# Performance work log

Measured on AMD Instinct MI355X. Metric: run time of the kernel, lower is better.

## Reference

```python
import jax, jax.numpy as jnp
import numpy as np

EPS_PROJ = 0.004   # float32 branch of _project
EPS_MIN = 1e-15


def _poincare_linear(x, weight_v, weight_g, bias, c):
    c = c.reshape(())
    rc = jnp.sqrt(c)
    # z_unit: column-normalized weight (weight_v / ||weight_v||_col)
    z_unit = weight_v / jnp.maximum(jnp.linalg.norm(weight_v, axis=0), EPS_MIN)  # [in, out]
    # unidirectional Poincare MLR
    drcr = 2.0 * rc * bias                                  # [out]
    rcx = rc * x                                            # [N, in]
    cx2 = jnp.sum(rcx * rcx, axis=-1, keepdims=True)        # [N, 1]
    num = 2.0 * (rcx @ z_unit) * jnp.cosh(drcr) - (1.0 + cx2) * jnp.sinh(drcr)
    mlr = 2.0 * weight_g / rc * jnp.arcsinh(num / jnp.maximum(1.0 - cx2, EPS_MIN))  # [N, out]
    # map back to the ball: sinh, then gyro-half map
    y = jnp.sinh(rc * mlr) / rc
    y = y / (1.0 + jnp.sqrt(1.0 + c * jnp.sum(y * y, axis=-1, keepdims=True)))
    # _project onto ball of curvature k = -c
    k = -c
    maxnorm = (1.0 - EPS_PROJ) / jnp.sqrt(jnp.maximum(jnp.abs(k), EPS_MIN))
    maxnorm = jnp.where(k < 0, maxnorm, jnp.float32(1e15))
    norm = jnp.maximum(jnp.linalg.norm(y, axis=-1, keepdims=True), EPS_MIN)
    return jnp.where(norm > maxnorm, y / norm * maxnorm, y)


def setup_inputs() -> dict:
    key = jax.random.key(0)
    k1, k2, k3 = jax.random.split(key, 3)
    N, IN, OUT = 32768, 1024, 1024
    # points strictly inside the unit Poincare ball (||x|| ~ 0.64)
    x = jax.random.normal(k1, (N, IN), dtype=jnp.float32) * 0.02
    std = (2.0 * IN * OUT) ** (-0.5)
    weight_v = jax.random.normal(k2, (IN, OUT), dtype=jnp.float32) * std
    weight_g = jax.random.uniform(k3, (OUT,), dtype=jnp.float32, minval=0.5, maxval=1.5) * std * (IN ** 0.5)
    bias = jnp.zeros((OUT,), dtype=jnp.float32)
    c = jnp.ones((1,), dtype=jnp.float32)
    return {"x": x, "weight_v": weight_v, "weight_g": weight_g, "bias": bias, "c": c}


def reference(x, weight_v, weight_g, bias, c):
    return _poincare_linear(x, weight_v, weight_g, bias, c)
```

## Files before the change

kernel.cpp:

```cpp
#include <hip/hip_runtime.h>

#define K_DIM 1024
#define N_DIM 1024

typedef short v8s __attribute__((ext_vector_type(8)));
typedef float v4f __attribute__((ext_vector_type(4)));

__device__ __forceinline__ unsigned int bf16_rne(float f) {
    unsigned int u = __float_as_uint(f);
    u += 0x7FFFu + ((u >> 16) & 1u);
    return u >> 16;
}

__global__ void sumsq_cols(const float* __restrict__ wv, float* __restrict__ colss) {
    __shared__ float red[4][64];
    const int t = threadIdx.x;
    const int cj = t & 63, rr = t >> 6;
    const int col = (blockIdx.x & 15) * 64 + cj;
    const int k0 = (blockIdx.x >> 4) * 128 + rr * 32;
    float ss = 0.f;
#pragma unroll 8
    for (int i = 0; i < 32; ++i) {
        float v = wv[(size_t)(k0 + i) * N_DIM + col];
        ss = fmaf(v, v, ss);
    }
    red[rr][cj] = ss;
    __syncthreads();
    if (rr == 0) atomicAdd(&colss[col], red[0][cj] + red[1][cj] + red[2][cj] + red[3][cj]);
}

__global__ void finalize_cols(const float* __restrict__ colss, const float* __restrict__ wg,
                              const float* __restrict__ bias, const float* __restrict__ cptr,
                              float* __restrict__ colinv, float* __restrict__ coshd,
                              float* __restrict__ sinhd, float* __restrict__ gfac) {
    const int col = blockIdx.x * 256 + threadIdx.x;
    const float rc = sqrtf(cptr[0]);
    colinv[col] = 1.0f / fmaxf(sqrtf(colss[col]), 1e-15f);
    float d = 2.0f * rc * bias[col];
    float e = __expf(d), ie = 1.0f / e;
    coshd[col] = 0.5f * (e + ie);
    sinhd[col] = 0.5f * (e - ie);
    gfac[col] = 2.0f * wg[col];
}

__global__ void build_bt(const float* __restrict__ wv, const float* __restrict__ colinv,
                         unsigned short* __restrict__ Btf) {
    __shared__ float tile[64 * 65];
    const int t = threadIdx.x;
    const int ti = blockIdx.x & 15;
    const int tj = blockIdx.x >> 4;
    {
        const int kl = t >> 2;
        const int cc = t & 3;
        const float* src = wv + (size_t)(ti * 64 + kl) * N_DIM + tj * 64 + cc * 16;
        float4 fq[4];
#pragma unroll
        for (int i = 0; i < 4; ++i) fq[i] = ((const float4*)src)[i];
        float* dst = &tile[kl * 65 + cc * 16];
#pragma unroll
        for (int i = 0; i < 4; ++i) {
            dst[4 * i + 0] = fq[i].x; dst[4 * i + 1] = fq[i].y;
            dst[4 * i + 2] = fq[i].z; dst[4 * i + 3] = fq[i].w;
        }
    }
    __syncthreads();
    {
        const int nl = t & 63, kc = t >> 6;
        const int n = tj * 64 + nl;
        const float ci = colinv[n];
        const int nt_g = tj * 4 + (nl >> 4);
#pragma unroll
        for (int h = 0; h < 2; ++h) {
            const int k8g = ti * 8 + kc * 2 + h;
            const int ks_g = k8g >> 2;
            const int L = (nl & 15) | ((k8g & 3) << 4);
            unsigned int p[4];
#pragma unroll
            for (int j = 0; j < 4; ++j) {
                float v0 = tile[(kc * 16 + h * 8 + 2 * j) * 65 + nl] * ci;
                float v1 = tile[(kc * 16 + h * 8 + 2 * j + 1) * 65 + nl] * ci;
                p[j] = bf16_rne(v0) | (bf16_rne(v1) << 16);
            }
            *(uint4*)(Btf + ((size_t)(nt_g * 32 + ks_g) * 64 + L) * 8) =
                make_uint4(p[0], p[1], p[2], p[3]);
        }
    }
}

__global__ void prep_a(const float* __restrict__ x, unsigned short* __restrict__ Axf,
                       float* __restrict__ rowss) {
    __shared__ float xs[16 * 1028];
    const int t = threadIdx.x;
    const int b = blockIdx.x;
    {
        const int r = t >> 4;
        const int c = t & 15;
        const float* xp = x + (size_t)(b * 16 + r) * K_DIM + c * 4;
        float* dst = &xs[r * 1028 + c * 4];
        float ss = 0.f;
#pragma unroll
        for (int it = 0; it < 16; ++it) {
            float4 v = *(const float4*)(xp + it * 64);
            ss = fmaf(v.x, v.x, ss); ss = fmaf(v.y, v.y, ss);
            ss = fmaf(v.z, v.z, ss); ss = fmaf(v.w, v.w, ss);
            *(float4*)(dst + it * 64) = v;
        }
        ss += __shfl_xor(ss, 1); ss += __shfl_xor(ss, 2);
        ss += __shfl_xor(ss, 4); ss += __shfl_xor(ss, 8);
        if (c == 0) rowss[b * 16 + r] = ss;
    }
    __syncthreads();
    {
        const int w = t >> 6, L = t & 63;
        const int lm = L & 15, q = L >> 4;
#pragma unroll
        for (int i = 0; i < 8; ++i) {
            const int ks = w * 8 + i;
            const float* src = &xs[lm * 1028 + ks * 32 + q * 8];
            float4 f0 = *(const float4*)(src);
            float4 f1 = *(const float4*)(src + 4);
            float vals[8] = {f0.x, f0.y, f0.z, f0.w, f1.x, f1.y, f1.z, f1.w};
            unsigned int p[4];
#pragma unroll
            for (int j = 0; j < 4; ++j)
                p[j] = bf16_rne(vals[2 * j]) | (bf16_rne(vals[2 * j + 1]) << 16);
            *(uint4*)(Axf + ((size_t)b * 32 + ks) * 512 + L * 8) =
                make_uint4(p[0], p[1], p[2], p[3]);
        }
    }
}

__launch_bounds__(256, 4)
__global__ void gemm_fast(const unsigned short* __restrict__ Axf,
                          const unsigned short* __restrict__ Btf,
                          const float* __restrict__ rowss, const float* __restrict__ cptr,
                          const float* __restrict__ coshd, const float* __restrict__ sinhd,
                          const float* __restrict__ gfac,
                          float* __restrict__ out, float* __restrict__ rowsum) {
    __shared__ __align__(16) unsigned short As[16 * 512];
    __shared__ __align__(16) unsigned short Bs[16 * 512];
    __shared__ float s_cx2[128];
    __shared__ float s_rsum[128];

    const int t = threadIdx.x;
    const int w = t >> 6, L = t & 63;
    const int lm = L & 15, q = L >> 4;
    const int bn = blockIdx.x & 7;
    const int bm = blockIdx.x >> 3;
    const int r0 = bm * 128;

    if (t < 128) { s_cx2[t] = rowss[r0 + t]; s_rsum[t] = 0.f; }

    v4f acc[16];
#pragma unroll
    for (int i = 0; i < 16; ++i) acc[i] = (v4f){0.f, 0.f, 0.f, 0.f};

    const int mt0 = w * 2;
    const int wm = w & 1, wn = w >> 1;

    for (int kq = 0; kq < 16; ++kq) {
#pragma unroll
        for (int i = 0; i < 4; ++i) {
            const int mtl = mt0 + (i & 1);
            const int ks = i >> 1;
            const unsigned short* gp =
                Axf + ((size_t)((bm * 8 + mtl) * 32) + (kq * 2 + ks)) * 512 + L * 8;
            __builtin_amdgcn_global_load_lds(
                (const __attribute__((address_space(1))) unsigned int*)gp,
                (__attribute__((address_space(3))) unsigned int*)&As[(mtl * 2 + ks) * 512],
                16, 0, 0);
        }
#pragma unroll
        for (int i = 0; i < 4; ++i) {
            const int nt = mt0 + (i & 1);
            const int ks = i >> 1;
            const unsigned short* gp =
                Btf + ((size_t)((bn * 8 + nt) * 32) + (kq * 2 + ks)) * 512 + L * 8;
            __builtin_amdgcn_global_load_lds(
                (const __attribute__((address_space(1))) unsigned int*)gp,
                (__attribute__((address_space(3))) unsigned int*)&Bs[(nt * 2 + ks) * 512],
                16, 0, 0);
        }
        __syncthreads();
#pragma unroll
        for (int ks = 0; ks < 2; ++ks) {
            v8s a[4], b[4];
#pragma unroll
            for (int mi = 0; mi < 4; ++mi)
                a[mi] = *(const v8s*)&As[((wm * 4 + mi) * 2 + ks) * 512 + L * 8];
#pragma unroll
            for (int ni = 0; ni < 4; ++ni)
                b[ni] = *(const v8s*)&Bs[((wn * 4 + ni) * 2 + ks) * 512 + L * 8];
#pragma unroll
            for (int mi = 0; mi < 4; ++mi)
#pragma unroll
                for (int ni = 0; ni < 4; ++ni)
                    acc[mi * 4 + ni] = __builtin_amdgcn_mfma_f32_16x16x32_bf16(
                        a[mi], b[ni], acc[mi * 4 + ni], 0, 0, 0);
        }
        __syncthreads();
    }

    const float cc = cptr[0];
    const float rc = sqrtf(cc);
    const float two_rc = 2.0f * rc;
    const float halfinvrc = 0.5f / rc;
    float ch[4], sh[4], gf[4];
#pragma unroll
    for (int ni = 0; ni < 4; ++ni) {
        const int n = bn * 128 + wn * 64 + ni * 16 + lm;
        ch[ni] = coshd[n]; sh[ni] = sinhd[n]; gf[ni] = gfac[n];
    }
#pragma unroll
    for (int mi = 0; mi < 4; ++mi) {
        const int mloc = wm * 64 + mi * 16 + q * 4;
        float sx[4];
#pragma unroll
        for (int rr = 0; rr < 4; ++rr) sx[rr] = cc * s_cx2[mloc + rr];
        float rs[4] = {0.f, 0.f, 0.f, 0.f};
#pragma unroll
        for (int ni = 0; ni < 4; ++ni) {
            v4f d = acc[mi * 4 + ni];
#pragma unroll
            for (int rr = 0; rr < 4; ++rr) {
                float cx2 = sx[rr];
                float num = two_rc * d[rr] * ch[ni] - (1.0f + cx2) * sh[ni];
                float den = fmaxf(1.0f - cx2, 1e-15f);
                float tt = num * __builtin_amdgcn_rcpf(den);
                float as_ = __logf(fabsf(tt) + sqrtf(fmaf(tt, tt, 1.0f)));
                as_ = copysignf(as_, tt);
                float u = gf[ni] * as_;
                float e = __expf(u);
                float y = (e - __builtin_amdgcn_rcpf(e)) * halfinvrc;
                d[rr] = y;
                rs[rr] = fmaf(y, y, rs[rr]);
            }
            acc[mi * 4 + ni] = d;
        }
#pragma unroll
        for (int rr = 0; rr < 4; ++rr) {
            float v = rs[rr];
            v += __shfl_xor(v, 1); v += __shfl_xor(v, 2);
            v += __shfl_xor(v, 4); v += __shfl_xor(v, 8);
            if (lm == 0) atomicAdd(&s_rsum[mloc + rr], v);
        }
#pragma unroll
        for (int rr = 0; rr < 4; ++rr) {
            const int row = r0 + mloc + rr;
            float* op = out + (size_t)row * N_DIM + bn * 128 + wn * 64 + lm;
#pragma unroll
            for (int ni = 0; ni < 4; ++ni) op[ni * 16] = acc[mi * 4 + ni][rr];
        }
    }
    __syncthreads();
    if (t < 128) atomicAdd(&rowsum[r0 + t], s_rsum[t]);
}

__launch_bounds__(256, 3)
__global__ void gemm_phase(const float* __restrict__ x, const unsigned short* __restrict__ Btf,
                           const float* __restrict__ cptr, const float* __restrict__ coshd,
                           const float* __restrict__ sinhd, const float* __restrict__ gfac,
                           float* __restrict__ out, float* __restrict__ rowsum) {
    __shared__ __align__(16) unsigned short As[16 * 512];
    __shared__ __align__(16) unsigned short Bs[16 * 512];
    __shared__ float s_cx2[128];
    __shared__ float s_rsum[128];

    const int t = threadIdx.x;
    const int w = t >> 6, L = t & 63;
    const int lm = L & 15, q = L >> 4;
    const int bn = blockIdx.x & 7;
    const int bm = blockIdx.x >> 3;
    const int r0 = bm * 128;

    if (t < 128) { s_cx2[t] = 0.f; s_rsum[t] = 0.f; }

    v4f acc[16];
#pragma unroll
    for (int i = 0; i < 16; ++i) acc[i] = (v4f){0.f, 0.f, 0.f, 0.f};

    const int smt0 = w * 2;
    const float* xr0 = x + (size_t)(r0 + smt0 * 16 + lm) * K_DIM;
    const float* xr1 = xr0 + (size_t)16 * K_DIM;
    float xp0 = 0.f, xp1 = 0.f;
    const int wm = w & 1, wn = w >> 1;

    for (int kq = 0; kq < 16; ++kq) {
        const int kbase = kq * 64;
#pragma unroll
        for (int i = 0; i < 4; ++i) {
            const int nt = smt0 + (i & 1);
            const int ks = i >> 1;
            const unsigned short* gp =
                Btf + ((size_t)((bn * 8 + nt) * 32 + (kq * 2 + ks)) * 64 + L) * 8;
            __builtin_amdgcn_global_load_lds(
                (const __attribute__((address_space(1))) unsigned int*)gp,
                (__attribute__((address_space(3))) unsigned int*)&Bs[(nt * 2 + ks) * 512],
                16, 0, 0);
        }
#pragma unroll
        for (int i = 0; i < 4; ++i) {
            const int half = i & 1;
            const int ks = i >> 1;
            const float* xr = half ? xr1 : xr0;
            const int kg = kbase + ks * 32 + q * 8;
            float4 f0 = *(const float4*)(xr + kg);
            float4 f1 = *(const float4*)(xr + kg + 4);
            float vals[8] = {f0.x, f0.y, f0.z, f0.w, f1.x, f1.y, f1.z, f1.w};
            unsigned int pk[4];
            float ssl = 0.f;
#pragma unroll
            for (int j = 0; j < 4; ++j) {
                ssl = fmaf(vals[2 * j], vals[2 * j], ssl);
                ssl = fmaf(vals[2 * j + 1], vals[2 * j + 1], ssl);
                pk[j] = bf16_rne(vals[2 * j]) | (bf16_rne(vals[2 * j + 1]) << 16);
            }
            if (half) xp1 += ssl; else xp0 += ssl;
            *(uint4*)&As[((smt0 + half) * 2 + ks) * 512 + L * 8] =
                make_uint4(pk[0], pk[1], pk[2], pk[3]);
        }
        __syncthreads();
#pragma unroll
        for (int ks = 0; ks < 2; ++ks) {
            v8s a[4], b[4];
#pragma unroll
            for (int mi = 0; mi < 4; ++mi)
                a[mi] = *(const v8s*)&As[((wm * 4 + mi) * 2 + ks) * 512 + L * 8];
#pragma unroll
            for (int ni = 0; ni < 4; ++ni)
                b[ni] = *(const v8s*)&Bs[((wn * 4 + ni) * 2 + ks) * 512 + L * 8];
#pragma unroll
            for (int mi = 0; mi < 4; ++mi)
#pragma unroll
                for (int ni = 0; ni < 4; ++ni)
                    acc[mi * 4 + ni] = __builtin_amdgcn_mfma_f32_16x16x32_bf16(
                        a[mi], b[ni], acc[mi * 4 + ni], 0, 0, 0);
        }
        __syncthreads();
    }

    atomicAdd(&s_cx2[smt0 * 16 + lm], xp0);
    atomicAdd(&s_cx2[smt0 * 16 + 16 + lm], xp1);
    __syncthreads();

    const float cc = cptr[0];
    const float rc = sqrtf(cc);
    const float two_rc = 2.0f * rc;
    const float halfinvrc = 0.5f / rc;
    float ch[4], sh[4], gf[4];
#pragma unroll
    for (int ni = 0; ni < 4; ++ni) {
        const int n = bn * 128 + wn * 64 + ni * 16 + lm;
        ch[ni] = coshd[n]; sh[ni] = sinhd[n]; gf[ni] = gfac[n];
    }
#pragma unroll
    for (int mi = 0; mi < 4; ++mi) {
        const int mloc = wm * 64 + mi * 16 + q * 4;
        float sx[4];
#pragma unroll
        for (int rr = 0; rr < 4; ++rr) sx[rr] = cc * s_cx2[mloc + rr];
        float rs[4] = {0.f, 0.f, 0.f, 0.f};
#pragma unroll
        for (int ni = 0; ni < 4; ++ni) {
            v4f d = acc[mi * 4 + ni];
#pragma unroll
            for (int rr = 0; rr < 4; ++rr) {
                float cx2 = sx[rr];
                float num = two_rc * d[rr] * ch[ni] - (1.0f + cx2) * sh[ni];
                float den = fmaxf(1.0f - cx2, 1e-15f);
                float tt = num * __builtin_amdgcn_rcpf(den);
                float as_ = __logf(fabsf(tt) + sqrtf(fmaf(tt, tt, 1.0f)));
                as_ = copysignf(as_, tt);
                float u = gf[ni] * as_;
                float e = __expf(u);
                float y = (e - __builtin_amdgcn_rcpf(e)) * halfinvrc;
                d[rr] = y;
                rs[rr] = fmaf(y, y, rs[rr]);
            }
            acc[mi * 4 + ni] = d;
        }
#pragma unroll
        for (int rr = 0; rr < 4; ++rr) {
            float v = rs[rr];
            v += __shfl_xor(v, 1); v += __shfl_xor(v, 2);
            v += __shfl_xor(v, 4); v += __shfl_xor(v, 8);
            if (lm == 0) atomicAdd(&s_rsum[mloc + rr], v);
        }
#pragma unroll
        for (int rr = 0; rr < 4; ++rr) {
            const int row = r0 + mloc + rr;
            float* op = out + (size_t)row * N_DIM + bn * 128 + wn * 64 + lm;
#pragma unroll
            for (int ni = 0; ni < 4; ++ni) op[ni * 16] = acc[mi * 4 + ni][rr];
        }
    }
    __syncthreads();
    if (t < 128) atomicAdd(&rowsum[r0 + t], s_rsum[t]);
}

__global__ void rescale(float* __restrict__ out, const float* __restrict__ rowsum,
                        const float* __restrict__ cptr) {
    const int t = threadIdx.x;
    const int row = blockIdx.x * 4 + (t >> 6);
    const float cc = cptr[0];
    const float s = rowsum[row];
    const float scale = 1.0f / (1.0f + sqrtf(fmaf(cc, s, 1.0f)));
    const float nrm = fmaxf(sqrtf(s) * scale, 1e-15f);
    const float mn = (cc > 0.f) ? 0.996f / sqrtf(fmaxf(cc, 1e-15f)) : 1e15f;
    const float f = scale * (nrm > mn ? mn / nrm : 1.0f);
    float4* p = (float4*)(out + (size_t)row * N_DIM) + (t & 63);
#pragma unroll
    for (int j = 0; j < 4; ++j) {
        float4 v = p[j * 64];
        v.x *= f; v.y *= f; v.z *= f; v.w *= f;
        p[j * 64] = v;
    }
}

extern "C" void kernel_launch(void* const* d_in, const int* in_sizes, int n_in,
                              void* d_out, int out_size, void* d_ws, size_t ws_size,
                              hipStream_t stream) {
    const float* x    = (const float*)d_in[0];
    const float* wv   = (const float*)d_in[1];
    const float* wg   = (const float*)d_in[2];
    const float* bias = (const float*)d_in[3];
    const float* cptr = (const float*)d_in[4];
    float* out = (float*)d_out;

    const int OUT = in_sizes[2];
    const int IN  = in_sizes[1] / OUT;
    const int M   = in_sizes[0] / IN;

    float* colss  = (float*)d_ws;
    float* rowsum = colss + 1024;
    float* rowss  = rowsum + M;
    float* colinv = rowss + M;
    float* coshd  = colinv + 1024;
    float* sinhd  = coshd + 1024;
    float* gfac   = sinhd + 1024;
    unsigned short* Btf = (unsigned short*)(gfac + 1024);
    unsigned short* Axf = Btf + (size_t)IN * OUT;

    const size_t need = (size_t)(1024 + 2 * M + 4096) * 4 + (size_t)IN * OUT * 2
                      + (size_t)M * IN * 2;

    hipMemsetAsync(rowsum, 0, (size_t)M * sizeof(float), stream);
    hipMemsetAsync(colss, 0, 1024 * sizeof(float), stream);
    sumsq_cols<<<128, 256, 0, stream>>>(wv, colss);
    finalize_cols<<<OUT / 256, 256, 0, stream>>>(colss, wg, bias, cptr, colinv, coshd, sinhd, gfac);
    build_bt<<<(IN / 64) * (OUT / 64), 256, 0, stream>>>(wv, colinv, Btf);
    if (ws_size >= need) {
        prep_a<<<M / 16, 256, 0, stream>>>(x, Axf, rowss);
        gemm_fast<<<(M / 128) * (OUT / 128), 256, 0, stream>>>(
            Axf, Btf, rowss, cptr, coshd, sinhd, gfac, out, rowsum);
    } else {
        gemm_phase<<<(M / 128) * (OUT / 128), 256, 0, stream>>>(
            x, Btf, cptr, coshd, sinhd, gfac, out, rowsum);
    }
    rescale<<<M / 4, 256, 0, stream>>>(out, rowsum, cptr);
}
```

Baseline: 385.4 us.

## Fuse row-norm rescale into GEMM with full-row tiles and register-streamed B

Replaces the 128x128-tile GEMM with a kernel where each 512-thread block owns 64 full rows across all 1024 output columns. The whole 64x1024 A tile is staged in LDS, and B fragments are streamed straight from global into registers with double buffering. Because each block now holds complete rows, the row sum of squares is reduced in LDS and the final gyro-half scaling and projection are applied before the store. This removes the rowsum memset, the global atomics and the separate rescale pass, which read and wrote the output a second time. In exchange it uses 128 KB of LDS and many accumulator registers per block, which limits occupancy, and B is re-read from global/L2 by every block.

```diff
diff --git a/kernel.cpp b/kernel.cpp
--- a/kernel.cpp
+++ b/kernel.cpp
@@ -130,13 +130,167 @@
     }
 }
 
-__launch_bounds__(256, 4)
-__global__ void gemm_fast(const unsigned short* __restrict__ Axf,
-                          const unsigned short* __restrict__ Btf,
-                          const float* __restrict__ rowss, const float* __restrict__ cptr,
-                          const float* __restrict__ coshd, const float* __restrict__ sinhd,
-                          const float* __restrict__ gfac,
-                          float* __restrict__ out, float* __restrict__ rowsum) {
+__launch_bounds__(512, 2)
+__global__ void gemm_fused(const unsigned short* __restrict__ Axf,
+                           const unsigned short* __restrict__ Btf,
+                           const float* __restrict__ rowss, const float* __restrict__ cptr,
+                           const float* __restrict__ coshd, const float* __restrict__ sinhd,
+                           const float* __restrict__ gfac,
+                           float* __restrict__ out) {
+    __shared__ __align__(16) unsigned short As[4 * 32 * 512];
+
+    const int t = threadIdx.x;
+    const int w = t >> 6, L = t & 63;
+    const int lm = L & 15, q = L >> 4;
+    const int bm = blockIdx.x;
+    const int r0 = bm * 64;
+
+    const unsigned short* ag = Axf + (size_t)bm * 65536;
+#pragma unroll
+    for (int r = 0; r < 16; ++r) {
+        __builtin_amdgcn_global_load_lds(
+            (const __attribute__((address_space(1))) unsigned int*)(ag + r * 4096 + t * 8),
+            (__attribute__((address_space(3))) unsigned int*)(As + r * 4096 + t * 8),
+            16, 0, 0);
+    }
+
+    const unsigned short* bw = Btf + (size_t)(w * 8) * 32 * 512 + (size_t)L * 8;
+
+    v4f acc[4][8];
+#pragma unroll
+    for (int i = 0; i < 4; ++i)
+#pragma unroll
+        for (int j = 0; j < 8; ++j) acc[i][j] = (v4f){0.f, 0.f, 0.f, 0.f};
+
+    v8s bA[8], bB[8];
+#pragma unroll
+    for (int n = 0; n < 8; ++n)
+        bA[n] = *(const v8s*)(bw + (n * 32) * 512);
+
+    __syncthreads();
+
+    const unsigned short* asw = As + L * 8;
+
+#pragma unroll 1
+    for (int kp = 0; kp < 16; ++kp) {
+        const int k0 = kp * 2;
+#pragma unroll
+        for (int n = 0; n < 8; ++n)
+            bB[n] = *(const v8s*)(bw + (n * 32 + k0 + 1) * 512);
+        {
+            v8s a[4];
+#pragma unroll
+            for (int mt = 0; mt < 4; ++mt)
+                a[mt] = *(const v8s*)(asw + (mt * 32 + k0) * 512);
+            __builtin_amdgcn_s_setprio(1);
+#pragma unroll
+            for (int mt = 0; mt < 4; ++mt)
+#pragma unroll
+                for (int n = 0; n < 8; ++n)
+                    acc[mt][n] = __builtin_amdgcn_mfma_f32_16x16x32_bf16(
+                        a[mt], bA[n], acc[mt][n], 0, 0, 0);
+            __builtin_amdgcn_s_setprio(0);
+        }
+        if (kp < 15) {
+#pragma unroll
+            for (int n = 0; n < 8; ++n)
+                bA[n] = *(const v8s*)(bw + (n * 32 + k0 + 2) * 512);
+        }
+        {
+            v8s a[4];
+#pragma unroll
+            for (int mt = 0; mt < 4; ++mt)
+                a[mt] = *(const v8s*)(asw + (mt * 32 + k0 + 1) * 512);
+            __builtin_amdgcn_s_setprio(1);
+#pragma unroll
+            for (int mt = 0; mt < 4; ++mt)
+#pragma unroll
+                for (int n = 0; n < 8; ++n)
+                    acc[mt][n] = __builtin_amdgcn_mfma_f32_16x16x32_bf16(
+                        a[mt], bB[n], acc[mt][n], 0, 0, 0);
+            __builtin_amdgcn_s_setprio(0);
+        }
+    }
+
+    float* s_rsum = (float*)As;
+
+    const float cc = cptr[0];
+    const float rc = sqrtf(cc);
+    const float two_rc = 2.0f * rc;
+    const float halfinvrc = 0.5f / rc;
+    float ch[8], sh[8], gf[8];
+#pragma unroll
+    for (int n = 0; n < 8; ++n) {
+        const int col = w * 128 + n * 16 + lm;
+        ch[n] = coshd[col]; sh[n] = sinhd[col]; gf[n] = gfac[col];
+    }
+
+    __syncthreads();
+    if (t < 64) s_rsum[t] = 0.f;
+    __syncthreads();
+
+#pragma unroll
+    for (int mt = 0; mt < 4; ++mt) {
+        const int mloc = mt * 16 + q * 4;
+        float sx[4];
+#pragma unroll
+        for (int rr = 0; rr < 4; ++rr) sx[rr] = cc * rowss[r0 + mloc + rr];
+        float rs[4] = {0.f, 0.f, 0.f, 0.f};
+#pragma unroll
+        for (int n = 0; n < 8; ++n) {
+            v4f d = acc[mt][n];
+#pragma unroll
+            for (int rr = 0; rr < 4; ++rr) {
+                float cx2 = sx[rr];
+                float num = two_rc * d[rr] * ch[n] - (1.0f + cx2) * sh[n];
+                float den = fmaxf(1.0f - cx2, 1e-15f);
+                float tt = num * __builtin_amdgcn_rcpf(den);
+                float as_ = __logf(fabsf(tt) + sqrtf(fmaf(tt, tt, 1.0f)));
+                as_ = copysignf(as_, tt);
+                float u = gf[n] * as_;
+                float e = __expf(u);
+                float y = (e - __builtin_amdgcn_rcpf(e)) * halfinvrc;
+                d[rr] = y;
+                rs[rr] = fmaf(y, y, rs[rr]);
+            }
+            acc[mt][n] = d;
+        }
+#pragma unroll
+        for (int rr = 0; rr < 4; ++rr) {
+            float v = rs[rr];
+            v += __shfl_xor(v, 1); v += __shfl_xor(v, 2);
+            v += __shfl_xor(v, 4); v += __shfl_xor(v, 8);
+            if (lm == 0) atomicAdd(&s_rsum[mloc + rr], v);
+        }
+    }
+    __syncthreads();
+
+    const float mn = (cc > 0.f) ? 0.996f / sqrtf(fmaxf(cc, 1e-15f)) : 1e15f;
+#pragma unroll
+    for (int mt = 0; mt < 4; ++mt) {
+        const int mloc = mt * 16 + q * 4;
+        float f[4];
+#pragma unroll
+        for (int rr = 0; rr < 4; ++rr) {
+            const float s = s_rsum[mloc + rr];
+            const float scale = 1.0f / (1.0f + sqrtf(fmaf(cc, s, 1.0f)));
+            const float nrm = fmaxf(sqrtf(s) * scale, 1e-15f);
+            f[rr] = scale * (nrm > mn ? mn / nrm : 1.0f);
+        }
+#pragma unroll
+        for (int rr = 0; rr < 4; ++rr) {
+            float* op = out + (size_t)(r0 + mloc + rr) * N_DIM + w * 128 + lm;
+#pragma unroll
+            for (int n = 0; n < 8; ++n) op[n * 16] = acc[mt][n][rr] * f[rr];
+        }
+    }
+}
+
+__launch_bounds__(256, 3)
+__global__ void gemm_phase(const float* __restrict__ x, const unsigned short* __restrict__ Btf,
+                           const float* __restrict__ cptr, const float* __restrict__ coshd,
+                           const float* __restrict__ sinhd, const float* __restrict__ gfac,
+                           float* __restrict__ out, float* __restrict__ rowsum) {
     __shared__ __align__(16) unsigned short As[16 * 512];
     __shared__ __align__(16) unsigned short Bs[16 * 512];
     __shared__ float s_cx2[128];
@@ -149,38 +303,52 @@
     const int bm = blockIdx.x >> 3;
     const int r0 = bm * 128;
 
-    if (t < 128) { s_cx2[t] = rowss[r0 + t]; s_rsum[t] = 0.f; }
+    if (t < 128) { s_cx2[t] = 0.f; s_rsum[t] = 0.f; }
 
     v4f acc[16];
 #pragma unroll
     for (int i = 0; i < 16; ++i) acc[i] = (v4f){0.f, 0.f, 0.f, 0.f};
 
-    const int mt0 = w * 2;
+    const int smt0 = w * 2;
+    const float* xr0 = x + (size_t)(r0 + smt0 * 16 + lm) * K_DIM;
+    const float* xr1 = xr0 + (size_t)16 * K_DIM;
+    float xp0 = 0.f, xp1 = 0.f;
     const int wm = w & 1, wn = w >> 1;
 
     for (int kq = 0; kq < 16; ++kq) {
+        const int kbase = kq * 64;
 #pragma unroll
         for (int i = 0; i < 4; ++i) {
-            const int mtl = mt0 + (i & 1);
+            const int nt = smt0 + (i & 1);
             const int ks = i >> 1;
             const unsigned short* gp =
-                Axf + ((size_t)((bm * 8 + mtl) * 32) + (kq * 2 + ks)) * 512 + L * 8;
-            __builtin_amdgcn_global_load_lds(
-                (const __attribute__((address_space(1))) unsigned int*)gp,
-                (__attribute__((address_space(3))) unsigned int*)&As[(mtl * 2 + ks) * 512],
-                16, 0, 0);
-        }
-#pragma unroll
-        for (int i = 0; i < 4; ++i) {
-            const int nt = mt0 + (i & 1);
-            const int ks = i >> 1;
-            const unsigned short* gp =
-                Btf + ((size_t)((bn * 8 + nt) * 32) + (kq * 2 + ks)) * 512 + L * 8;
+                Btf + ((size_t)((bn * 8 + nt) * 32 + (kq * 2 + ks)) * 64 + L) * 8;
             __builtin_amdgcn_global_load_lds(
                 (const __attribute__((address_space(1))) unsigned int*)gp,
                 (__attribute__((address_space(3))) unsigned int*)&Bs[(nt * 2 + ks) * 512],
                 16, 0, 0);
         }
+#pragma unroll
+        for (int i = 0; i < 4; ++i) {
+            const int half = i & 1;
+            const int ks = i >> 1;
+            const float* xr = half ? xr1 : xr0;
+            const int kg = kbase + ks * 32 + q * 8;
+            float4 f0 = *(const float4*)(xr + kg);
+            float4 f1 = *(const float4*)(xr + kg + 4);
+            float vals[8] = {f0.x, f0.y, f0.z, f0.w, f1.x, f1.y, f1.z, f1.w};
+            unsigned int pk[4];
+            float ssl = 0.f;
+#pragma unroll
+            for (int j = 0; j < 4; ++j) {
+                ssl = fmaf(vals[2 * j], vals[2 * j], ssl);
+                ssl = fmaf(vals[2 * j + 1], vals[2 * j + 1], ssl);
+                pk[j] = bf16_rne(vals[2 * j]) | (bf16_rne(vals[2 * j + 1]) << 16);
+            }
+            if (half) xp1 += ssl; else xp0 += ssl;
+            *(uint4*)&As[((smt0 + half) * 2 + ks) * 512 + L * 8] =
+                make_uint4(pk[0], pk[1], pk[2], pk[3]);
+        }
         __syncthreads();
 #pragma unroll
         for (int ks = 0; ks < 2; ++ks) {
@@ -200,6 +368,10 @@
         }
         __syncthreads();
     }
+
+    atomicAdd(&s_cx2[smt0 * 16 + lm], xp0);
+    atomicAdd(&s_cx2[smt0 * 16 + 16 + lm], xp1);
+    __syncthreads();
 
     const float cc = cptr[0];
     const float rc = sqrtf(cc);
@@ -256,148 +428,6 @@
     if (t < 128) atomicAdd(&rowsum[r0 + t], s_rsum[t]);
 }
 
-__launch_bounds__(256, 3)
-__global__ void gemm_phase(const float* __restrict__ x, const unsigned short* __restrict__ Btf,
-                           const float* __restrict__ cptr, const float* __restrict__ coshd,
-                           const float* __restrict__ sinhd, const float* __restrict__ gfac,
-                           float* __restrict__ out, float* __restrict__ rowsum) {
-    __shared__ __align__(16) unsigned short As[16 * 512];
-    __shared__ __align__(16) unsigned short Bs[16 * 512];
-    __shared__ float s_cx2[128];
-    __shared__ float s_rsum[128];
-
-    const int t = threadIdx.x;
-    const int w = t >> 6, L = t & 63;
-    const int lm = L & 15, q = L >> 4;
-    const int bn = blockIdx.x & 7;
-    const int bm = blockIdx.x >> 3;
-    const int r0 = bm * 128;
-
-    if (t < 128) { s_cx2[t] = 0.f; s_rsum[t] = 0.f; }
-
-    v4f acc[16];
-#pragma unroll
-    for (int i = 0; i < 16; ++i) acc[i] = (v4f){0.f, 0.f, 0.f, 0.f};
-
-    const int smt0 = w * 2;
-    const float* xr0 = x + (size_t)(r0 + smt0 * 16 + lm) * K_DIM;
-    const float* xr1 = xr0 + (size_t)16 * K_DIM;
-    float xp0 = 0.f, xp1 = 0.f;
-    const int wm = w & 1, wn = w >> 1;
-
-    for (int kq = 0; kq < 16; ++kq) {
-        const int kbase = kq * 64;
-#pragma unroll
-        for (int i = 0; i < 4; ++i) {
-            const int nt = smt0 + (i & 1);
-            const int ks = i >> 1;
-            const unsigned short* gp =
-                Btf + ((size_t)((bn * 8 + nt) * 32 + (kq * 2 + ks)) * 64 + L) * 8;
-            __builtin_amdgcn_global_load_lds(
-                (const __attribute__((address_space(1))) unsigned int*)gp,
-                (__attribute__((address_space(3))) unsigned int*)&Bs[(nt * 2 + ks) * 512],
-                16, 0, 0);
-        }
-#pragma unroll
-        for (int i = 0; i < 4; ++i) {
-            const int half = i & 1;
-            const int ks = i >> 1;
-            const float* xr = half ? xr1 : xr0;
-            const int kg = kbase + ks * 32 + q * 8;
-            float4 f0 = *(const float4*)(xr + kg);
-            float4 f1 = *(const float4*)(xr + kg + 4);
-            float vals[8] = {f0.x, f0.y, f0.z, f0.w, f1.x, f1.y, f1.z, f1.w};
-            unsigned int pk[4];
-            float ssl = 0.f;
-#pragma unroll
-            for (int j = 0; j < 4; ++j) {
-                ssl = fmaf(vals[2 * j], vals[2 * j], ssl);
-                ssl = fmaf(vals[2 * j + 1], vals[2 * j + 1], ssl);
-                pk[j] = bf16_rne(vals[2 * j]) | (bf16_rne(vals[2 * j + 1]) << 16);
-            }
-            if (half) xp1 += ssl; else xp0 += ssl;
-            *(uint4*)&As[((smt0 + half) * 2 + ks) * 512 + L * 8] =
-                make_uint4(pk[0], pk[1], pk[2], pk[3]);
-        }
-        __syncthreads();
-#pragma unroll
-        for (int ks = 0; ks < 2; ++ks) {
-            v8s a[4], b[4];
-#pragma unroll
-            for (int mi = 0; mi < 4; ++mi)
-                a[mi] = *(const v8s*)&As[((wm * 4 + mi) * 2 + ks) * 512 + L * 8];
-#pragma unroll
-            for (int ni = 0; ni < 4; ++ni)
-                b[ni] = *(const v8s*)&Bs[((wn * 4 + ni) * 2 + ks) * 512 + L * 8];
-#pragma unroll
-            for (int mi = 0; mi < 4; ++mi)
-#pragma unroll
-                for (int ni = 0; ni < 4; ++ni)
-                    acc[mi * 4 + ni] = __builtin_amdgcn_mfma_f32_16x16x32_bf16(
-                        a[mi], b[ni], acc[mi * 4 + ni], 0, 0, 0);
-        }
-        __syncthreads();
-    }
-
-    atomicAdd(&s_cx2[smt0 * 16 + lm], xp0);
-    atomicAdd(&s_cx2[smt0 * 16 + 16 + lm], xp1);
-    __syncthreads();
-
-    const float cc = cptr[0];
-    const float rc = sqrtf(cc);
-    const float two_rc = 2.0f * rc;
-    const float halfinvrc = 0.5f / rc;
-    float ch[4], sh[4], gf[4];
-#pragma unroll
-    for (int ni = 0; ni < 4; ++ni) {
-        const int n = bn * 128 + wn * 64 + ni * 16 + lm;
-        ch[ni] = coshd[n]; sh[ni] = sinhd[n]; gf[ni] = gfac[n];
-    }
-#pragma unroll
-    for (int mi = 0; mi < 4; ++mi) {
-        const int mloc = wm * 64 + mi * 16 + q * 4;
-        float sx[4];
-#pragma unroll
-        for (int rr = 0; rr < 4; ++rr) sx[rr] = cc * s_cx2[mloc + rr];
-        float rs[4] = {0.f, 0.f, 0.f, 0.f};
-#pragma unroll
-        for (int ni = 0; ni < 4; ++ni) {
-            v4f d = acc[mi * 4 + ni];
-#pragma unroll
-            for (int rr = 0; rr < 4; ++rr) {
-                float cx2 = sx[rr];
-                float num = two_rc * d[rr] * ch[ni] - (1.0f + cx2) * sh[ni];
-                float den = fmaxf(1.0f - cx2, 1e-15f);
-                float tt = num * __builtin_amdgcn_rcpf(den);
-                float as_ = __logf(fabsf(tt) + sqrtf(fmaf(tt, tt, 1.0f)));
-                as_ = copysignf(as_, tt);
-                float u = gf[ni] * as_;
-                float e = __expf(u);
-                float y = (e - __builtin_amdgcn_rcpf(e)) * halfinvrc;
-                d[rr] = y;
-                rs[rr] = fmaf(y, y, rs[rr]);
-            }
-            acc[mi * 4 + ni] = d;
-        }
-#pragma unroll
-        for (int rr = 0; rr < 4; ++rr) {
-            float v = rs[rr];
-            v += __shfl_xor(v, 1); v += __shfl_xor(v, 2);
-            v += __shfl_xor(v, 4); v += __shfl_xor(v, 8);
-            if (lm == 0) atomicAdd(&s_rsum[mloc + rr], v);
-        }
-#pragma unroll
-        for (int rr = 0; rr < 4; ++rr) {
-            const int row = r0 + mloc + rr;
-            float* op = out + (size_t)row * N_DIM + bn * 128 + wn * 64 + lm;
-#pragma unroll
-            for (int ni = 0; ni < 4; ++ni) op[ni * 16] = acc[mi * 4 + ni][rr];
-        }
-    }
-    __syncthreads();
-    if (t < 128) atomicAdd(&rowsum[r0 + t], s_rsum[t]);
-}
-
 __global__ void rescale(float* __restrict__ out, const float* __restrict__ rowsum,
                         const float* __restrict__ cptr) {
     const int t = threadIdx.x;
@@ -444,18 +474,18 @@
     const size_t need = (size_t)(1024 + 2 * M + 4096) * 4 + (size_t)IN * OUT * 2
                       + (size_t)M * IN * 2;
 
-    hipMemsetAsync(rowsum, 0, (size_t)M * sizeof(float), stream);
     hipMemsetAsync(colss, 0, 1024 * sizeof(float), stream);
     sumsq_cols<<<128, 256, 0, stream>>>(wv, colss);
     finalize_cols<<<OUT / 256, 256, 0, stream>>>(colss, wg, bias, cptr, colinv, coshd, sinhd, gfac);
     build_bt<<<(IN / 64) * (OUT / 64), 256, 0, stream>>>(wv, colinv, Btf);
     if (ws_size >= need) {
         prep_a<<<M / 16, 256, 0, stream>>>(x, Axf, rowss);
-        gemm_fast<<<(M / 128) * (OUT / 128), 256, 0, stream>>>(
-            Axf, Btf, rowss, cptr, coshd, sinhd, gfac, out, rowsum);
+        gemm_fused<<<M / 64, 512, 0, stream>>>(
+            Axf, Btf, rowss, cptr, coshd, sinhd, gfac, out);
     } else {
+        hipMemsetAsync(rowsum, 0, (size_t)M * sizeof(float), stream);
         gemm_phase<<<(M / 128) * (OUT / 128), 256, 0, stream>>>(
             x, Btf, cptr, coshd, sinhd, gfac, out, rowsum);
-    }
-    rescale<<<M / 4, 256, 0, stream>>>(out, rowsum, cptr);
-}
+        rescale<<<M / 4, 256, 0, stream>>>(out, rowsum, cptr);
+    }
+}
```

Result: faster. 362.3 us (-6.0%).
